# Kernel optimization log

Hardware: AMD Instinct MI355X
Metric: run time of the kernel (lower is better)

## Reference

```python
import jax, jax.numpy as jnp
import numpy as np

B, N, T, D, M, HOPS = 32, 300, 12, 64, 16, 2

def setup_inputs() -> dict:
    key = jax.random.key(0)
    ks = jax.random.split(key, 12)
    inp = {
        "X": jax.random.normal(ks[0], (B, D, N, T), dtype=jnp.float32),
        "timeEmbedding": jax.random.normal(ks[1], (B, N, T, D), dtype=jnp.float32),
        "adjW": jax.random.normal(ks[2], (N, D), dtype=jnp.float32) * (1.0 / np.sqrt(D)),
        "adjB": jnp.zeros((N,), dtype=jnp.float32),
        "trainW1": jax.random.normal(ks[3], (N, M), dtype=jnp.float32) * 0.1,
        "trainW2": jax.random.normal(ks[4], (M, D * D), dtype=jnp.float32) * 0.1,
        "alpha1": jax.random.normal(ks[5], (N, M), dtype=jnp.float32) * 0.1,
        "alpha2": jax.random.normal(ks[6], (M, N), dtype=jnp.float32) * 0.1,
        "beta1": jax.random.normal(ks[7], (N, M), dtype=jnp.float32) * 0.1,
        "beta2": jax.random.normal(ks[8], (M, N), dtype=jnp.float32) * 0.1,
        "gcnW": jax.random.normal(ks[9], (D, D * (HOPS + 1)), dtype=jnp.float32) * (1.0 / np.sqrt(D * (HOPS + 1))),
        "gcnB": jnp.zeros((D,), dtype=jnp.float32),
    }
    return inp

def reference(X, timeEmbedding, adjW, adjB, trainW1, trainW2, alpha1, alpha2, beta1, beta2, gcnW, gcnB):
    # timeEmbedding: [B,N,T,D] -> [B,T,N,D]
    te = jnp.transpose(timeEmbedding, (0, 2, 1, 3))
    # learned adjacency: A[b,t,n,k]
    A = jnp.sin(jnp.einsum('btnd,kd->btnk', te, adjW) + adjB)  # Linear(dmodel->N)
    A = (alpha1 @ alpha2) * A            # elementwise scale by [N,N], broadcast over b,t
    A = jax.nn.relu(A + beta1 @ beta2)
    # X: [B,D,N,T] -> [B,T,N,D]
    Xp = jnp.transpose(X, (0, 3, 2, 1))
    # per-node weight matrices [N,D,D]
    W = (trainW1 @ trainW2).reshape(N, D, D)
    Hs = [Xp]
    Hb = Xp
    for _ in range(HOPS):
        Hnow = jnp.einsum('btnk,btkd->btnd', A, Hb)      # adjacency aggregation
        Hnow = jnp.einsum('btnk,nkd->btnd', Hnow, W)     # per-node distinct matmul
        pre = Xp + Hnow
        Hnow = jax.nn.sigmoid(pre) * jnp.tanh(pre)        # gated residual
        Hs.append(Hnow)
        Hb = Hnow
    H = jnp.concatenate(Hs, axis=3)                       # [B,T,N,D*(hops+1)]
    Hout = jnp.einsum('btnf,df->btnd', H, gcnW) + gcnB    # gcnLinear (dropout = identity in eval)
    return jnp.transpose(Hout, (0, 3, 2, 1))              # [B,D,N,T]
```

## Files before the change

### kernel.cpp

```cpp
#include <hip/hip_runtime.h>

#define Nq 300
#define Tq 12
#define Dq 64
#define Mq 16
#define BTq 384
#define DDq (Dq*Dq)
#define Fq (Dq*3)
#define NP 320

typedef short bf8_t __attribute__((ext_vector_type(8)));
typedef float f4_t  __attribute__((ext_vector_type(4)));

__device__ __forceinline__ unsigned short f2bf(float f) {
    unsigned u = __float_as_uint(f);
    u = (u + 0x7FFFu + ((u >> 16) & 1u)) >> 16;
    return (unsigned short)u;
}
__device__ __forceinline__ float bf2f(unsigned short u) {
    return __uint_as_float((unsigned)u << 16);
}
__device__ __forceinline__ float4 ld4(const float* p) { return *(const float4*)p; }

__device__ __forceinline__ bf8_t pack8(float4 a, float4 b) {
    bf8_t r;
    r[0] = (short)f2bf(a.x); r[1] = (short)f2bf(a.y);
    r[2] = (short)f2bf(a.z); r[3] = (short)f2bf(a.w);
    r[4] = (short)f2bf(b.x); r[5] = (short)f2bf(b.y);
    r[6] = (short)f2bf(b.z); r[7] = (short)f2bf(b.w);
    return r;
}

__device__ __forceinline__ float gatef(float p) {
    float pc = fminf(fmaxf(p, -30.f), 30.f);
    float sig = 1.f / (1.f + __expf(-pc));
    float e2  = __expf(2.f * pc);
    float th  = (e2 - 1.f) / (e2 + 1.f);
    return sig * th;
}

__global__ void __launch_bounds__(256) kprep_all(
    const float* __restrict__ a1, const float* __restrict__ a2,
    const float* __restrict__ b1, const float* __restrict__ b2,
    const float* __restrict__ w1, const float* __restrict__ w2,
    const float* __restrict__ adjW, const float* __restrict__ adjB,
    const float* __restrict__ X,
    unsigned* __restrict__ ABt, unsigned short* __restrict__ Wt,
    unsigned short* __restrict__ adjWb, float* __restrict__ adjBp,
    unsigned short* __restrict__ Xp_t, unsigned short* __restrict__ Xp_nb)
{
    __shared__ char smem[64 * 308 * 2];
    const int vb = blockIdx.x;
    const int tid = threadIdx.x;

    if (vb < 400) {
        const int tile = vb;
        const int reg = tid & 3, lane = tid >> 2;
        const int nt = tile % 5;  int r1 = tile / 5;
        const int w  = r1 % 4;    int r2 = r1 / 4;
        const int c  = r2 % 5;    const int qi = r2 / 5;
        const int n = qi*80 + nt*16 + (lane & 15);
        const int k = c*64 + w*16 + (lane >> 4)*4 + reg;
        unsigned outv = 0u;
        if (n < Nq && k < Nq) {
            float sa = 0.f, sb = 0.f;
            #pragma unroll
            for (int m = 0; m < Mq; ++m) {
                sa = fmaf(a1[n*Mq+m], a2[m*Nq+k], sa);
                sb = fmaf(b1[n*Mq+m], b2[m*Nq+k], sb);
            }
            outv = ((unsigned)f2bf(sb) << 16) | (unsigned)f2bf(sa);
        }
        ABt[tile*256 + tid] = outv;
    } else if (vb < 700) {
        float* sT = (float*)smem;
        __shared__ float sw1[Mq];
        const int n = vb - 400;
        if (tid < Mq) sw1[tid] = w1[n*Mq + tid];
        __syncthreads();
        for (int i = tid; i < DDq; i += 256) {
            int k = i >> 6, d = i & 63;
            float s = 0.f;
            #pragma unroll
            for (int m = 0; m < Mq; ++m) s = fmaf(sw1[m], w2[m*DDq + i], s);
            sT[d*65 + k] = s;
        }
        __syncthreads();
        for (int i = tid; i < DDq; i += 256) {
            int d = i >> 6, k = i & 63;
            Wt[(size_t)n*DDq + i] = f2bf(sT[d*65 + k]);
        }
    } else if (vb < 780) {
        int e = (vb - 700) * 256 + tid;
        if (e < NP * 64) {
            int k = e >> 6, d = e & 63;
            adjWb[e] = (k < Nq) ? f2bf(adjW[k*Dq + d]) : (unsigned short)0;
        }
        if (e < NP) adjBp[e] = (e < Nq) ? adjB[e] : 0.f;
    } else {
        unsigned short* sT = (unsigned short*)smem;
        const int bx = vb - 780;
        const int b = bx / 12, tile = bx % 12;
        const int n0 = tile * 25;
        for (int i = tid; i < 64 * 300; i += 256) {
            int d = i / 300, j = i - d * 300;
            sT[d*308 + j] = f2bf(X[(size_t)(b*64 + d)*3600 + n0*12 + j]);
        }
        __syncthreads();
        for (int wi = tid; wi < 12 * 64 * 25; wi += 256) {
            int nl = wi % 25, rem = wi / 25;
            int d = rem % 64, t = rem / 64;
            Xp_t[((size_t)(b*Tq + t)*64 + d)*NP + n0 + nl] = sT[d*308 + nl*12 + t];
        }
        if (tile == 11) {
            for (int wi = tid; wi < 12 * 64 * 20; wi += 256) {
                int e = wi % 20, rem = wi / 20;
                int d = rem % 64, t = rem / 64;
                Xp_t[((size_t)(b*Tq + t)*64 + d)*NP + 300 + e] = 0;
            }
        }
        for (int wi = tid; wi < 25 * 12 * 64; wi += 256) {
            int d = wi & 63, rem = wi >> 6;
            int t = rem % 12, nl = rem / 12;
            Xp_nb[((size_t)(n0 + nl)*BTq + b*Tq + t)*64 + d] = sT[d*308 + nl*12 + t];
        }
    }
}

__global__ void __launch_bounds__(256) ktr2(const unsigned short* __restrict__ Hnb,
                                            unsigned short* __restrict__ Ht) {
    __shared__ unsigned short sT[64 * 308];
    const int bt = blockIdx.x;
    const int tid = threadIdx.x;
    for (int i = tid; i < 300 * 64; i += 256) {
        int n = i >> 6, d = i & 63;
        sT[d*308 + n] = Hnb[((size_t)n*BTq + bt)*64 + d];
    }
    __syncthreads();
    for (int wi = tid; wi < 64 * 80; wi += 256) {
        int kq = wi % 80, d = wi / 80;
        ushort4 o;
        int k = kq * 4;
        o.x = (k+0 < Nq) ? sT[d*308 + k+0] : (unsigned short)0;
        o.y = (k+1 < Nq) ? sT[d*308 + k+1] : (unsigned short)0;
        o.z = (k+2 < Nq) ? sT[d*308 + k+2] : (unsigned short)0;
        o.w = (k+3 < Nq) ? sT[d*308 + k+3] : (unsigned short)0;
        *(ushort4*)&Ht[((size_t)bt*64 + d)*NP + k] = o;
    }
}

__global__ void __launch_bounds__(256) kfuse(
    const float* __restrict__ te,
    const unsigned short* __restrict__ adjWb,
    const float* __restrict__ adjBp,
    const unsigned* __restrict__ ABt,
    const unsigned short* __restrict__ Hb_t,
    unsigned short* __restrict__ Hout_nb)
{
    __shared__ unsigned short sPl[2][80 * 72];
    const int bt = blockIdx.x >> 2, qi = blockIdx.x & 3;
    const int b = bt / Tq, t = bt - b * Tq;
    const int nbase = qi * 80;
    const int tid = threadIdx.x;
    const int w = tid >> 6, lane = tid & 63, quad = lane >> 4, l16 = lane & 15;
    const int dcol = w*16 + l16;

    bf8_t tb0[5], tb1[5];
    #pragma unroll
    for (int nt = 0; nt < 5; ++nt) {
        int n = nbase + nt*16 + l16; if (n > Nq-1) n = Nq-1;
        const float* ter = te + (((size_t)b*Nq + n)*Tq + t)*Dq;
        tb0[nt] = pack8(ld4(ter + quad*8),      ld4(ter + quad*8 + 4));
        tb1[nt] = pack8(ld4(ter + 32 + quad*8), ld4(ter + 36 + quad*8));
    }
    f4_t accO[5];
    #pragma unroll
    for (int rt = 0; rt < 5; ++rt) accO[rt] = (f4_t){0.f, 0.f, 0.f, 0.f};

    for (int c = 0; c < 5; ++c) {
        const int cbase = c * 64;
        const unsigned short* ar = adjWb + (cbase + w*16 + l16)*64;
        bf8_t ka0 = *(const bf8_t*)(ar + quad*8);
        bf8_t ka1 = *(const bf8_t*)(ar + 32 + quad*8);
        float4 bias4 = ld4(adjBp + cbase + w*16 + quad*4);
        const unsigned* abbase = ABt + ((((size_t)qi*5 + c)*4 + w)*5)*256 + lane*4;
        unsigned short* sp = sPl[c & 1];
        #pragma unroll
        for (int nt = 0; nt < 5; ++nt) {
            f4_t p = {0.f, 0.f, 0.f, 0.f};
            p = __builtin_amdgcn_mfma_f32_16x16x32_bf16(ka0, tb0[nt], p, 0, 0, 0);
            p = __builtin_amdgcn_mfma_f32_16x16x32_bf16(ka1, tb1[nt], p, 0, 0, 0);
            uint4 ab = *(const uint4*)(abbase + nt*256);
            ushort4 o4;
            {
                float sv = __sinf(p[0] + bias4.x);
                o4.x = f2bf(fmaxf(fmaf(__uint_as_float(ab.x << 16), sv,
                                       __uint_as_float(ab.x & 0xFFFF0000u)), 0.f));
            }
            {
                float sv = __sinf(p[1] + bias4.y);
                o4.y = f2bf(fmaxf(fmaf(__uint_as_float(ab.y << 16), sv,
                                       __uint_as_float(ab.y & 0xFFFF0000u)), 0.f));
            }
            {
                float sv = __sinf(p[2] + bias4.z);
                o4.z = f2bf(fmaxf(fmaf(__uint_as_float(ab.z << 16), sv,
                                       __uint_as_float(ab.z & 0xFFFF0000u)), 0.f));
            }
            {
                float sv = __sinf(p[3] + bias4.w);
                o4.w = f2bf(fmaxf(fmaf(__uint_as_float(ab.w << 16), sv,
                                       __uint_as_float(ab.w & 0xFFFF0000u)), 0.f));
            }
            *(ushort4*)&sp[(nt*16 + l16)*72 + w*16 + quad*4] = o4;
        }
        __syncthreads();
        const unsigned short* hr = Hb_t + ((size_t)bt*64 + dcol)*NP + cbase;
        bf8_t v0 = *(const bf8_t*)(hr + quad*8);
        bf8_t v1 = *(const bf8_t*)(hr + 32 + quad*8);
        #pragma unroll
        for (int rt = 0; rt < 5; ++rt) {
            bf8_t p0 = *(const bf8_t*)&sp[(rt*16 + l16)*72 + quad*8];
            bf8_t p1 = *(const bf8_t*)&sp[(rt*16 + l16)*72 + 32 + quad*8];
            accO[rt] = __builtin_amdgcn_mfma_f32_16x16x32_bf16(p0, v0, accO[rt], 0, 0, 0);
            accO[rt] = __builtin_amdgcn_mfma_f32_16x16x32_bf16(p1, v1, accO[rt], 0, 0, 0);
        }
    }
    #pragma unroll
    for (int rt = 0; rt < 5; ++rt) {
        #pragma unroll
        for (int reg = 0; reg < 4; ++reg) {
            int ng = nbase + rt*16 + quad*4 + reg;
            if (ng < Nq)
                Hout_nb[((size_t)ng*BTq + bt)*64 + dcol] = f2bf(accO[rt][reg]);
        }
    }
}

__global__ void __launch_bounds__(256) kmm(
    const unsigned short* __restrict__ Hagg_nb,
    const unsigned short* __restrict__ Xp_nb,
    const unsigned short* __restrict__ Wt,
    unsigned short* __restrict__ Hout_nb)
{
    const int n = blockIdx.x >> 2, qi = blockIdx.x & 3;
    const int bt0 = qi * 96;
    const int tid = threadIdx.x;
    const int w = tid >> 6, lane = tid & 63, quad = lane >> 4, l16 = lane & 15;
    const int dcol = w*16 + l16;
    const unsigned short* wn = Wt + (size_t)n * DDq + dcol*64;
    bf8_t v0 = *(const bf8_t*)(wn + quad*8);
    bf8_t v1 = *(const bf8_t*)(wn + 32 + quad*8);
    f4_t acc[6];
    #pragma unroll
    for (int rt = 0; rt < 6; ++rt) acc[rt] = (f4_t){0.f, 0.f, 0.f, 0.f};
    #pragma unroll
    for (int rt = 0; rt < 6; ++rt) {
        int r = bt0 + rt*16 + l16;
        const unsigned short* row = Hagg_nb + ((size_t)n*BTq + r)*64;
        bf8_t a0 = *(const bf8_t*)(row + quad*8);
        bf8_t a1 = *(const bf8_t*)(row + 32 + quad*8);
        acc[rt] = __builtin_amdgcn_mfma_f32_16x16x32_bf16(a0, v0, acc[rt], 0, 0, 0);
        acc[rt] = __builtin_amdgcn_mfma_f32_16x16x32_bf16(a1, v1, acc[rt], 0, 0, 0);
    }
    __syncthreads();
    #pragma unroll
    for (int rt = 0; rt < 6; ++rt) {
        #pragma unroll
        for (int reg = 0; reg < 4; ++reg) {
            int r = bt0 + rt*16 + quad*4 + reg;
            size_t idx = ((size_t)n*BTq + r)*64 + dcol;
            float xp = bf2f(Xp_nb[idx]);
            Hout_nb[idx] = f2bf(gatef(xp + acc[rt][reg]));
        }
    }
}

__global__ void __launch_bounds__(256) kgcn(
    const unsigned short* __restrict__ Xp_nb, const unsigned short* __restrict__ H1_nb,
    const unsigned short* __restrict__ H2_nb, const float* __restrict__ gcnW,
    const float* __restrict__ gcnB, float* __restrict__ out)
{
    const int b = blockIdx.x / 19, tile = blockIdx.x % 19;
    const int n0 = tile * 16;
    const int rows = (tile == 18) ? 144 : 192;
    const int tid = threadIdx.x;
    const int w = tid >> 6, lane = tid & 63, quad = lane >> 4, l16 = lane & 15;
    const int dcol = w*16 + l16;
    const float bias = gcnB[dcol];
    f4_t acc[12];
    #pragma unroll
    for (int rt = 0; rt < 12; ++rt) acc[rt] = (f4_t){0.f, 0.f, 0.f, 0.f};
    const unsigned short* bufs[3] = {Xp_nb, H1_nb, H2_nb};
    #pragma unroll
    for (int c = 0; c < 3; ++c) {
        const unsigned short* buf = bufs[c];
        const float* gwr = gcnW + (size_t)dcol*Fq + c*Dq;
        bf8_t v0 = pack8(ld4(gwr + quad*8),      ld4(gwr + quad*8 + 4));
        bf8_t v1 = pack8(ld4(gwr + 32 + quad*8), ld4(gwr + 36 + quad*8));
        #pragma unroll
        for (int rt = 0; rt < 12; ++rt) {
            int r = rt*16 + l16;
            int nl = r / 12, t = r - nl*12;
            int n = n0 + nl; if (n > Nq-1) n = Nq-1;
            const unsigned short* row = buf + ((size_t)n*BTq + b*Tq + t)*64;
            bf8_t a0 = *(const bf8_t*)(row + quad*8);
            bf8_t a1 = *(const bf8_t*)(row + 32 + quad*8);
            acc[rt] = __builtin_amdgcn_mfma_f32_16x16x32_bf16(a0, v0, acc[rt], 0, 0, 0);
            acc[rt] = __builtin_amdgcn_mfma_f32_16x16x32_bf16(a1, v1, acc[rt], 0, 0, 0);
        }
    }
    float* outd = out + (size_t)(b*Dq + dcol)*3600 + n0*12;
    #pragma unroll
    for (int rt = 0; rt < 12; ++rt) {
        if (rt*16 < rows) {
            int r0 = rt*16 + quad*4;
            float4 o = make_float4(acc[rt][0] + bias, acc[rt][1] + bias,
                                   acc[rt][2] + bias, acc[rt][3] + bias);
            *(float4*)&outd[r0] = o;
        }
    }
}

extern "C" void kernel_launch(void* const* d_in, const int* in_sizes, int n_in,
                              void* d_out, int out_size, void* d_ws, size_t ws_size,
                              hipStream_t stream) {
    (void)in_sizes; (void)n_in; (void)out_size; (void)ws_size;
    const float* X    = (const float*)d_in[0];
    const float* te   = (const float*)d_in[1];
    const float* adjW = (const float*)d_in[2];
    const float* adjB = (const float*)d_in[3];
    const float* w1   = (const float*)d_in[4];
    const float* w2   = (const float*)d_in[5];
    const float* a1   = (const float*)d_in[6];
    const float* a2   = (const float*)d_in[7];
    const float* b1   = (const float*)d_in[8];
    const float* b2   = (const float*)d_in[9];
    const float* gW   = (const float*)d_in[10];
    const float* gB   = (const float*)d_in[11];
    float* out = (float*)d_out;

    char* ws = (char*)d_ws;
    unsigned*       ABt    = (unsigned*)      (ws);
    unsigned short* adjWb  = (unsigned short*)(ws + 409600);
    float*          adjBp  = (float*)         (ws + 450560);
    unsigned short* Wt     = (unsigned short*)(ws + 451840);
    unsigned short* Xp_t   = (unsigned short*)(ws + 2909440);
    unsigned short* Xp_nb  = (unsigned short*)(ws + 18638080);
    unsigned short* Hagg   = (unsigned short*)(ws + 33383680);
    unsigned short* H1_nb  = (unsigned short*)(ws + 48129280);
    unsigned short* H1_t   = (unsigned short*)(ws + 62874880);

    hipLaunchKernelGGL(kprep_all, dim3(1164), dim3(256), 0, stream,
                       a1, a2, b1, b2, w1, w2, adjW, adjB, X,
                       ABt, Wt, adjWb, adjBp, Xp_t, Xp_nb);
    hipLaunchKernelGGL(kfuse, dim3(1536), dim3(256), 0, stream, te, adjWb, adjBp, ABt, Xp_t, Hagg);
    hipLaunchKernelGGL(kmm,   dim3(1200), dim3(256), 0, stream, Hagg, Xp_nb, Wt, H1_nb);
    hipLaunchKernelGGL(ktr2,  dim3(384),  dim3(256), 0, stream, H1_nb, H1_t);
    hipLaunchKernelGGL(kfuse, dim3(1536), dim3(256), 0, stream, te, adjWb, adjBp, ABt, H1_t, Hagg);
    hipLaunchKernelGGL(kmm,   dim3(1200), dim3(256), 0, stream, Hagg, Xp_nb, Wt, Hagg);
    hipLaunchKernelGGL(kgcn,  dim3(608), dim3(256), 0, stream, Xp_nb, H1_nb, Hagg, gW, gB, out);
}
```

Measured before the change: 322.9 us.

## Vectorize transposes, cache bf16 time embedding, prefetch operands, split gcn rows

Several independent changes land together. The X transpose is split across twice as many blocks and now uses float4 loads and ushort4 stores. kfuse becomes a template: hop 1 writes a bf16 copy of the time embedding and hop 2 reads it back instead of re-reading fp32. It also prefetches the next H chunk and the AB values, and swaps MFMA operands so outputs store as ushort4 vectors. kmm loads its rows before the MFMAs and stores vectorised, ktr2 reads ushort4, and kgcn splits its rows over three times as many blocks for more parallelism. The cost is extra workspace, higher register pressure, and more kprep blocks.

```diff
diff --git a/kernel.cpp b/kernel.cpp
--- a/kernel.cpp
+++ b/kernel.cpp
@@ -100,29 +100,38 @@
     } else {
         unsigned short* sT = (unsigned short*)smem;
         const int bx = vb - 780;
-        const int b = bx / 12, tile = bx % 12;
-        const int n0 = tile * 25;
-        for (int i = tid; i < 64 * 300; i += 256) {
-            int d = i / 300, j = i - d * 300;
-            sT[d*308 + j] = f2bf(X[(size_t)(b*64 + d)*3600 + n0*12 + j]);
+        const int b = bx / 24, sub = bx % 24;
+        const int tile = sub >> 1, half = sub & 1;
+        const int n0 = tile * 25, d0 = half * 32;
+        for (int i = tid; i < 32 * 75; i += 256) {
+            int dl = i / 75, jq = i - dl*75, j = jq*4;
+            float4 v = ld4(&X[(size_t)(b*64 + d0 + dl)*3600 + n0*12 + j]);
+            ushort4 o;
+            o.x = f2bf(v.x); o.y = f2bf(v.y); o.z = f2bf(v.z); o.w = f2bf(v.w);
+            *(ushort4*)&sT[dl*308 + j] = o;
         }
         __syncthreads();
-        for (int wi = tid; wi < 12 * 64 * 25; wi += 256) {
+        for (int wi = tid; wi < 12 * 32 * 25; wi += 256) {
             int nl = wi % 25, rem = wi / 25;
-            int d = rem % 64, t = rem / 64;
-            Xp_t[((size_t)(b*Tq + t)*64 + d)*NP + n0 + nl] = sT[d*308 + nl*12 + t];
+            int dl = rem & 31, t = rem >> 5;
+            Xp_t[((size_t)(b*Tq + t)*64 + d0 + dl)*NP + n0 + nl] = sT[dl*308 + nl*12 + t];
         }
         if (tile == 11) {
-            for (int wi = tid; wi < 12 * 64 * 20; wi += 256) {
+            for (int wi = tid; wi < 12 * 32 * 20; wi += 256) {
                 int e = wi % 20, rem = wi / 20;
-                int d = rem % 64, t = rem / 64;
-                Xp_t[((size_t)(b*Tq + t)*64 + d)*NP + 300 + e] = 0;
-            }
-        }
-        for (int wi = tid; wi < 25 * 12 * 64; wi += 256) {
-            int d = wi & 63, rem = wi >> 6;
+                int dl = rem & 31, t = rem >> 5;
+                Xp_t[((size_t)(b*Tq + t)*64 + d0 + dl)*NP + 300 + e] = 0;
+            }
+        }
+        for (int wi = tid; wi < 25 * 12 * 8; wi += 256) {
+            int dg = wi & 7, rem = wi >> 3;
             int t = rem % 12, nl = rem / 12;
-            Xp_nb[((size_t)(n0 + nl)*BTq + b*Tq + t)*64 + d] = sT[d*308 + nl*12 + t];
+            ushort4 o;
+            o.x = sT[(dg*4+0)*308 + nl*12 + t];
+            o.y = sT[(dg*4+1)*308 + nl*12 + t];
+            o.z = sT[(dg*4+2)*308 + nl*12 + t];
+            o.w = sT[(dg*4+3)*308 + nl*12 + t];
+            *(ushort4*)&Xp_nb[((size_t)(n0+nl)*BTq + b*Tq + t)*64 + d0 + dg*4] = o;
         }
     }
 }
@@ -132,9 +141,13 @@
     __shared__ unsigned short sT[64 * 308];
     const int bt = blockIdx.x;
     const int tid = threadIdx.x;
-    for (int i = tid; i < 300 * 64; i += 256) {
-        int n = i >> 6, d = i & 63;
-        sT[d*308 + n] = Hnb[((size_t)n*BTq + bt)*64 + d];
+    for (int i = tid; i < 300 * 16; i += 256) {
+        int nl = i >> 4, dg = i & 15;
+        ushort4 v = *(const ushort4*)&Hnb[((size_t)nl*BTq + bt)*64 + dg*4];
+        sT[(dg*4+0)*308 + nl] = v.x;
+        sT[(dg*4+1)*308 + nl] = v.y;
+        sT[(dg*4+2)*308 + nl] = v.z;
+        sT[(dg*4+3)*308 + nl] = v.w;
     }
     __syncthreads();
     for (int wi = tid; wi < 64 * 80; wi += 256) {
@@ -149,8 +162,10 @@
     }
 }
 
-__global__ void __launch_bounds__(256) kfuse(
+template<int HOP>
+__global__ void __launch_bounds__(256) kfuse_t(
     const float* __restrict__ te,
+    unsigned short* __restrict__ teP,
     const unsigned short* __restrict__ adjWb,
     const float* __restrict__ adjBp,
     const unsigned* __restrict__ ABt,
@@ -169,28 +184,50 @@
     #pragma unroll
     for (int nt = 0; nt < 5; ++nt) {
         int n = nbase + nt*16 + l16; if (n > Nq-1) n = Nq-1;
-        const float* ter = te + (((size_t)b*Nq + n)*Tq + t)*Dq;
-        tb0[nt] = pack8(ld4(ter + quad*8),      ld4(ter + quad*8 + 4));
-        tb1[nt] = pack8(ld4(ter + 32 + quad*8), ld4(ter + 36 + quad*8));
+        if (HOP == 1) {
+            const float* ter = te + (((size_t)b*Nq + n)*Tq + t)*Dq;
+            tb0[nt] = pack8(ld4(ter + quad*8),      ld4(ter + quad*8 + 4));
+            tb1[nt] = pack8(ld4(ter + 32 + quad*8), ld4(ter + 36 + quad*8));
+            if (w == 0) {
+                *(bf8_t*)&teP[((size_t)bt*Nq + n)*64 + quad*8] = tb0[nt];
+                *(bf8_t*)&teP[((size_t)bt*Nq + n)*64 + 32 + quad*8] = tb1[nt];
+            }
+        } else {
+            const unsigned short* tr = teP + ((size_t)bt*Nq + n)*64;
+            tb0[nt] = *(const bf8_t*)(tr + quad*8);
+            tb1[nt] = *(const bf8_t*)(tr + 32 + quad*8);
+        }
     }
     f4_t accO[5];
     #pragma unroll
     for (int rt = 0; rt < 5; ++rt) accO[rt] = (f4_t){0.f, 0.f, 0.f, 0.f};
+
+    const unsigned short* hr = Hb_t + ((size_t)bt*64 + dcol)*NP;
+    bf8_t hv0 = *(const bf8_t*)(hr + quad*8);
+    bf8_t hv1 = *(const bf8_t*)(hr + 32 + quad*8);
 
     for (int c = 0; c < 5; ++c) {
         const int cbase = c * 64;
+        bf8_t nhv0, nhv1;
+        if (c < 4) {
+            nhv0 = *(const bf8_t*)(hr + cbase + 64 + quad*8);
+            nhv1 = *(const bf8_t*)(hr + cbase + 96 + quad*8);
+        }
+        const unsigned* abbase = ABt + ((((size_t)qi*5 + c)*4 + w)*5)*256 + lane*4;
+        uint4 abv[5];
+        #pragma unroll
+        for (int nt = 0; nt < 5; ++nt) abv[nt] = *(const uint4*)(abbase + nt*256);
         const unsigned short* ar = adjWb + (cbase + w*16 + l16)*64;
         bf8_t ka0 = *(const bf8_t*)(ar + quad*8);
         bf8_t ka1 = *(const bf8_t*)(ar + 32 + quad*8);
         float4 bias4 = ld4(adjBp + cbase + w*16 + quad*4);
-        const unsigned* abbase = ABt + ((((size_t)qi*5 + c)*4 + w)*5)*256 + lane*4;
         unsigned short* sp = sPl[c & 1];
         #pragma unroll
         for (int nt = 0; nt < 5; ++nt) {
             f4_t p = {0.f, 0.f, 0.f, 0.f};
             p = __builtin_amdgcn_mfma_f32_16x16x32_bf16(ka0, tb0[nt], p, 0, 0, 0);
             p = __builtin_amdgcn_mfma_f32_16x16x32_bf16(ka1, tb1[nt], p, 0, 0, 0);
-            uint4 ab = *(const uint4*)(abbase + nt*256);
+            uint4 ab = abv[nt];
             ushort4 o4;
             {
                 float sv = __sinf(p[0] + bias4.x);
@@ -215,24 +252,23 @@
             *(ushort4*)&sp[(nt*16 + l16)*72 + w*16 + quad*4] = o4;
         }
         __syncthreads();
-        const unsigned short* hr = Hb_t + ((size_t)bt*64 + dcol)*NP + cbase;
-        bf8_t v0 = *(const bf8_t*)(hr + quad*8);
-        bf8_t v1 = *(const bf8_t*)(hr + 32 + quad*8);
         #pragma unroll
         for (int rt = 0; rt < 5; ++rt) {
             bf8_t p0 = *(const bf8_t*)&sp[(rt*16 + l16)*72 + quad*8];
             bf8_t p1 = *(const bf8_t*)&sp[(rt*16 + l16)*72 + 32 + quad*8];
-            accO[rt] = __builtin_amdgcn_mfma_f32_16x16x32_bf16(p0, v0, accO[rt], 0, 0, 0);
-            accO[rt] = __builtin_amdgcn_mfma_f32_16x16x32_bf16(p1, v1, accO[rt], 0, 0, 0);
-        }
+            accO[rt] = __builtin_amdgcn_mfma_f32_16x16x32_bf16(hv0, p0, accO[rt], 0, 0, 0);
+            accO[rt] = __builtin_amdgcn_mfma_f32_16x16x32_bf16(hv1, p1, accO[rt], 0, 0, 0);
+        }
+        if (c < 4) { hv0 = nhv0; hv1 = nhv1; }
     }
     #pragma unroll
     for (int rt = 0; rt < 5; ++rt) {
-        #pragma unroll
-        for (int reg = 0; reg < 4; ++reg) {
-            int ng = nbase + rt*16 + quad*4 + reg;
-            if (ng < Nq)
-                Hout_nb[((size_t)ng*BTq + bt)*64 + dcol] = f2bf(accO[rt][reg]);
+        int n = nbase + rt*16 + l16;
+        if (n < Nq) {
+            ushort4 o;
+            o.x = f2bf(accO[rt][0]); o.y = f2bf(accO[rt][1]);
+            o.z = f2bf(accO[rt][2]); o.w = f2bf(accO[rt][3]);
+            *(ushort4*)&Hout_nb[((size_t)n*BTq + bt)*64 + w*16 + quad*4] = o;
         }
     }
 }
@@ -251,28 +287,38 @@
     const unsigned short* wn = Wt + (size_t)n * DDq + dcol*64;
     bf8_t v0 = *(const bf8_t*)(wn + quad*8);
     bf8_t v1 = *(const bf8_t*)(wn + 32 + quad*8);
-    f4_t acc[6];
-    #pragma unroll
-    for (int rt = 0; rt < 6; ++rt) acc[rt] = (f4_t){0.f, 0.f, 0.f, 0.f};
+    bf8_t a0[6], a1[6];
     #pragma unroll
     for (int rt = 0; rt < 6; ++rt) {
         int r = bt0 + rt*16 + l16;
         const unsigned short* row = Hagg_nb + ((size_t)n*BTq + r)*64;
-        bf8_t a0 = *(const bf8_t*)(row + quad*8);
-        bf8_t a1 = *(const bf8_t*)(row + 32 + quad*8);
-        acc[rt] = __builtin_amdgcn_mfma_f32_16x16x32_bf16(a0, v0, acc[rt], 0, 0, 0);
-        acc[rt] = __builtin_amdgcn_mfma_f32_16x16x32_bf16(a1, v1, acc[rt], 0, 0, 0);
+        a0[rt] = *(const bf8_t*)(row + quad*8);
+        a1[rt] = *(const bf8_t*)(row + 32 + quad*8);
+    }
+    f4_t acc[6];
+    #pragma unroll
+    for (int rt = 0; rt < 6; ++rt) acc[rt] = (f4_t){0.f, 0.f, 0.f, 0.f};
+    #pragma unroll
+    for (int rt = 0; rt < 6; ++rt) {
+        acc[rt] = __builtin_amdgcn_mfma_f32_16x16x32_bf16(v0, a0[rt], acc[rt], 0, 0, 0);
+        acc[rt] = __builtin_amdgcn_mfma_f32_16x16x32_bf16(v1, a1[rt], acc[rt], 0, 0, 0);
     }
     __syncthreads();
+    ushort4 xp4[6];
     #pragma unroll
     for (int rt = 0; rt < 6; ++rt) {
-        #pragma unroll
-        for (int reg = 0; reg < 4; ++reg) {
-            int r = bt0 + rt*16 + quad*4 + reg;
-            size_t idx = ((size_t)n*BTq + r)*64 + dcol;
-            float xp = bf2f(Xp_nb[idx]);
-            Hout_nb[idx] = f2bf(gatef(xp + acc[rt][reg]));
-        }
+        int r = bt0 + rt*16 + l16;
+        xp4[rt] = *(const ushort4*)&Xp_nb[((size_t)n*BTq + r)*64 + w*16 + quad*4];
+    }
+    #pragma unroll
+    for (int rt = 0; rt < 6; ++rt) {
+        int r = bt0 + rt*16 + l16;
+        ushort4 o;
+        o.x = f2bf(gatef(bf2f(xp4[rt].x) + acc[rt][0]));
+        o.y = f2bf(gatef(bf2f(xp4[rt].y) + acc[rt][1]));
+        o.z = f2bf(gatef(bf2f(xp4[rt].z) + acc[rt][2]));
+        o.w = f2bf(gatef(bf2f(xp4[rt].w) + acc[rt][3]));
+        *(ushort4*)&Hout_nb[((size_t)n*BTq + r)*64 + w*16 + quad*4] = o;
     }
 }
 
@@ -281,16 +327,19 @@
     const unsigned short* __restrict__ H2_nb, const float* __restrict__ gcnW,
     const float* __restrict__ gcnB, float* __restrict__ out)
 {
-    const int b = blockIdx.x / 19, tile = blockIdx.x % 19;
+    const int bid = blockIdx.x;
+    const int b = bid / 57, rem = bid % 57;
+    const int tile = rem / 3, rg = rem % 3;
     const int n0 = tile * 16;
     const int rows = (tile == 18) ? 144 : 192;
+    const int r0base = rg * 64;
     const int tid = threadIdx.x;
     const int w = tid >> 6, lane = tid & 63, quad = lane >> 4, l16 = lane & 15;
     const int dcol = w*16 + l16;
     const float bias = gcnB[dcol];
-    f4_t acc[12];
-    #pragma unroll
-    for (int rt = 0; rt < 12; ++rt) acc[rt] = (f4_t){0.f, 0.f, 0.f, 0.f};
+    f4_t acc[4];
+    #pragma unroll
+    for (int rt = 0; rt < 4; ++rt) acc[rt] = (f4_t){0.f, 0.f, 0.f, 0.f};
     const unsigned short* bufs[3] = {Xp_nb, H1_nb, H2_nb};
     #pragma unroll
     for (int c = 0; c < 3; ++c) {
@@ -299,22 +348,26 @@
         bf8_t v0 = pack8(ld4(gwr + quad*8),      ld4(gwr + quad*8 + 4));
         bf8_t v1 = pack8(ld4(gwr + 32 + quad*8), ld4(gwr + 36 + quad*8));
         #pragma unroll
-        for (int rt = 0; rt < 12; ++rt) {
-            int r = rt*16 + l16;
-            int nl = r / 12, t = r - nl*12;
-            int n = n0 + nl; if (n > Nq-1) n = Nq-1;
-            const unsigned short* row = buf + ((size_t)n*BTq + b*Tq + t)*64;
-            bf8_t a0 = *(const bf8_t*)(row + quad*8);
-            bf8_t a1 = *(const bf8_t*)(row + 32 + quad*8);
-            acc[rt] = __builtin_amdgcn_mfma_f32_16x16x32_bf16(a0, v0, acc[rt], 0, 0, 0);
-            acc[rt] = __builtin_amdgcn_mfma_f32_16x16x32_bf16(a1, v1, acc[rt], 0, 0, 0);
+        for (int rt = 0; rt < 4; ++rt) {
+            int rr = r0base + rt*16;
+            if (rr < rows) {
+                int r = rr + l16;
+                int nl = r / 12, t = r - nl*12;
+                int n = n0 + nl; if (n > Nq-1) n = Nq-1;
+                const unsigned short* row = buf + ((size_t)n*BTq + b*Tq + t)*64;
+                bf8_t a0 = *(const bf8_t*)(row + quad*8);
+                bf8_t a1 = *(const bf8_t*)(row + 32 + quad*8);
+                acc[rt] = __builtin_amdgcn_mfma_f32_16x16x32_bf16(a0, v0, acc[rt], 0, 0, 0);
+                acc[rt] = __builtin_amdgcn_mfma_f32_16x16x32_bf16(a1, v1, acc[rt], 0, 0, 0);
+            }
         }
     }
     float* outd = out + (size_t)(b*Dq + dcol)*3600 + n0*12;
     #pragma unroll
-    for (int rt = 0; rt < 12; ++rt) {
-        if (rt*16 < rows) {
-            int r0 = rt*16 + quad*4;
+    for (int rt = 0; rt < 4; ++rt) {
+        int rr = r0base + rt*16;
+        if (rr < rows) {
+            int r0 = rr + quad*4;
             float4 o = make_float4(acc[rt][0] + bias, acc[rt][1] + bias,
                                    acc[rt][2] + bias, acc[rt][3] + bias);
             *(float4*)&outd[r0] = o;
@@ -350,14 +403,17 @@
     unsigned short* Hagg   = (unsigned short*)(ws + 33383680);
     unsigned short* H1_nb  = (unsigned short*)(ws + 48129280);
     unsigned short* H1_t   = (unsigned short*)(ws + 62874880);
-
-    hipLaunchKernelGGL(kprep_all, dim3(1164), dim3(256), 0, stream,
+    unsigned short* teP    = (unsigned short*)(ws + 78603520);
+
+    hipLaunchKernelGGL(kprep_all, dim3(1548), dim3(256), 0, stream,
                        a1, a2, b1, b2, w1, w2, adjW, adjB, X,
                        ABt, Wt, adjWb, adjBp, Xp_t, Xp_nb);
-    hipLaunchKernelGGL(kfuse, dim3(1536), dim3(256), 0, stream, te, adjWb, adjBp, ABt, Xp_t, Hagg);
+    hipLaunchKernelGGL(HIP_KERNEL_NAME(kfuse_t<1>), dim3(1536), dim3(256), 0, stream,
+                       te, teP, adjWb, adjBp, ABt, Xp_t, Hagg);
     hipLaunchKernelGGL(kmm,   dim3(1200), dim3(256), 0, stream, Hagg, Xp_nb, Wt, H1_nb);
     hipLaunchKernelGGL(ktr2,  dim3(384),  dim3(256), 0, stream, H1_nb, H1_t);
-    hipLaunchKernelGGL(kfuse, dim3(1536), dim3(256), 0, stream, te, adjWb, adjBp, ABt, H1_t, Hagg);
+    hipLaunchKernelGGL(HIP_KERNEL_NAME(kfuse_t<2>), dim3(1536), dim3(256), 0, stream,
+                       te, teP, adjWb, adjBp, ABt, H1_t, Hagg);
     hipLaunchKernelGGL(kmm,   dim3(1200), dim3(256), 0, stream, Hagg, Xp_nb, Wt, Hagg);
-    hipLaunchKernelGGL(kgcn,  dim3(608), dim3(256), 0, stream, Xp_nb, H1_nb, Hagg, gW, gB, out);
-}
+    hipLaunchKernelGGL(kgcn,  dim3(1824), dim3(256), 0, stream, Xp_nb, H1_nb, Hagg, gW, gB, out);
+}
```

After: 295.9 us. 8.3% less time.
